# Optimization experiments

Hardware: AMD Instinct MI355X
Metric: run time of the kernel (lower is better)

The kernel has to match this reference:

```python
import jax, jax.numpy as jnp
import numpy as np

B1, B2, D = 8192, 8192, 128


def _cdist(d1, d2):
    # L2 distance matrix via the |a|^2 + |b|^2 - 2ab expansion (GEMM-dominant).
    d1_sq = jnp.sum(d1 * d1, axis=1, keepdims=True)          # (B1, 1)
    d2_sq = jnp.sum(d2 * d2, axis=1, keepdims=True)          # (B2, 1)
    dm = d1_sq + d2_sq.T - 2.0 * (d1 @ d2.T)                 # (B1, B2)
    return jnp.sqrt(jnp.clip(dm, 0.0))


def setup_inputs() -> dict:
    key = jax.random.key(0)
    k1, k2 = jax.random.split(key)
    desc1 = jax.random.normal(k1, (B1, D), dtype=jnp.float32)
    desc2 = jax.random.normal(k2, (B2, D), dtype=jnp.float32)
    return {"desc1": desc1, "desc2": desc2}


def reference(desc1, desc2):
    # DescriptorMatcher(match_mode='nn'): nearest neighbor in desc2 for each desc1.
    dm = _cdist(desc1, desc2)                                # (B1, B2)
    idxs_in_2 = jnp.argmin(dm, axis=1)                       # (B1,)
    match_dists = jnp.take_along_axis(dm, idxs_in_2[:, None], axis=1)  # (B1, 1)
    idxs_in_1 = jnp.arange(dm.shape[0], dtype=jnp.int64 if jax.config.jax_enable_x64 else jnp.int32)
    matches_idxs = jnp.stack([idxs_in_1, idxs_in_2.astype(idxs_in_1.dtype)], axis=1)  # (B1, 2)
    return match_dists, matches_idxs
```

## Files before the change

kernel.cpp:

```cpp
#include <hip/hip_runtime.h>
#include <cstdint>

#define NB1 8192
#define NB2 8192
#define DDIM 128
#define KROW 256
#define NKITER 12

using half8   = __attribute__((ext_vector_type(8))) _Float16;
using half4   = __attribute__((ext_vector_type(4))) _Float16;
using float4v = __attribute__((ext_vector_type(4))) float;

typedef __attribute__((address_space(3))) void       lds_void;
typedef const __attribute__((address_space(1))) void glb_void;

__device__ inline unsigned long long packkey(float v, int j) {
  unsigned u = __float_as_uint(v);
  u = (u & 0x80000000u) ? ~u : (u | 0x80000000u);
  return ((unsigned long long)u << 32) | (unsigned)j;
}

__device__ __forceinline__ int a_src(int kt) { return (kt < 8) ? kt : kt - 8; }
__device__ __forceinline__ int b_src(int kt) { return (kt < 4) ? kt : kt - 4; }

__global__ __launch_bounds__(256) void convert_kernel(
    const float* __restrict__ d1, const float* __restrict__ d2,
    _Float16* __restrict__ A2, _Float16* __restrict__ B2,
    float* __restrict__ asq, float* __restrict__ bsq,
    unsigned long long* __restrict__ packed) {
  int gid  = blockIdx.x * 256 + threadIdx.x;
  int wv   = gid >> 6;
  int lane = gid & 63;
  int rowc = 2 * wv + (lane >> 5);
  bool isA = rowc < NB1;
  const float* src = isA ? d1 : d2;
  int row = isA ? rowc : rowc - NB1;
  int k4  = (lane & 31) * 4;

  float4 v = *(const float4*)&src[row * DDIM + k4];
  _Float16 h0 = (_Float16)v.x, h1 = (_Float16)v.y;
  _Float16 h2 = (_Float16)v.z, h3 = (_Float16)v.w;
  half4 hh = {h0, h1, h2, h3};
  half4 ll = {(_Float16)(v.x - (float)h0), (_Float16)(v.y - (float)h1),
              (_Float16)(v.z - (float)h2), (_Float16)(v.w - (float)h3)};

  _Float16* dst = (isA ? A2 : B2) + (size_t)row * KROW;
  *(half4*)&dst[k4]       = hh;
  *(half4*)&dst[128 + k4] = ll;

  float s = v.x * v.x + v.y * v.y + v.z * v.z + v.w * v.w;
  #pragma unroll
  for (int off = 16; off > 0; off >>= 1) s += __shfl_xor(s, off, 64);
  if ((lane & 31) == 0) (isA ? asq : bsq)[row] = s;

  if (gid < NB1) packed[gid] = 0xFFFFFFFFFFFFFFFFull;
}

__global__ __launch_bounds__(256, 3) void mfma_match_kernel(
    const _Float16* __restrict__ A2, const _Float16* __restrict__ B2,
    const float* __restrict__ bsq, unsigned long long* __restrict__ packed) {
  __shared__ unsigned long long smem[2 * 128 * 17];
  _Float16* Asb = (_Float16*)smem;
  _Float16* Bsb = (_Float16*)smem + 8192;

  const int t    = threadIdx.x;
  const int lane = t & 63;
  const int wid  = t >> 6;
  const int wm = wid >> 1, wn = wid & 1;
  const int lx = lane & 15, q = lane >> 4;

  const int id = blockIdx.x;
  const int xc = id & 7, kk = id >> 3;
  const int bx = ((kk >> 3) & 7) * 8 + xc;
  const int by = (kk & 7) + ((kk >> 6) & 7) * 8;
  const int row0 = bx * 128, col0 = by * 128;

  const int sA   = wid * 2;
  const int rloc = lane >> 2;
  const int qch  = ((lane & 3) - (rloc >> 1)) & 3;
  const int rA0  = sA * 16 + rloc;
  const int kofs = qch * 8;

  float4v acc[4][4];
  #pragma unroll
  for (int r = 0; r < 4; ++r)
    #pragma unroll
    for (int c = 0; c < 4; ++c) acc[r][c] = (float4v){0.f, 0.f, 0.f, 0.f};

  float bq[4]; int jc[4];
  #pragma unroll
  for (int c = 0; c < 4; ++c) {
    jc[c] = col0 + wn * 64 + 16 * c + lx;
    bq[c] = bsq[jc[c]];
  }

  auto stage = [&](int kt, int buf) {
    const _Float16* ga =
        A2 + (size_t)(row0 + rA0) * KROW + a_src(kt) * 32 + kofs;
    __builtin_amdgcn_global_load_lds((glb_void*)ga,
        (lds_void*)(Asb + buf * 4096 + sA * 512), 16, 0, 0);
    __builtin_amdgcn_global_load_lds((glb_void*)(ga + 16 * KROW),
        (lds_void*)(Asb + buf * 4096 + (sA + 1) * 512), 16, 0, 0);
    const _Float16* gb =
        B2 + (size_t)(col0 + rA0) * KROW + b_src(kt) * 32 + kofs;
    __builtin_amdgcn_global_load_lds((glb_void*)gb,
        (lds_void*)(Bsb + buf * 4096 + sA * 512), 16, 0, 0);
    __builtin_amdgcn_global_load_lds((glb_void*)(gb + 16 * KROW),
        (lds_void*)(Bsb + buf * 4096 + (sA + 1) * 512), 16, 0, 0);
  };

  stage(0, 0);

  const int sw = ((q + (lx >> 1)) & 3) * 8;

  #pragma unroll
  for (int kt = 0; kt < NKITER; ++kt) {
    __syncthreads();
    if (kt < NKITER - 1) stage(kt + 1, (kt + 1) & 1);
    const _Float16* Ab = Asb + (kt & 1) * 4096;
    const _Float16* Bb = Bsb + (kt & 1) * 4096;
    half8 af[4], bf[4];
    #pragma unroll
    for (int r = 0; r < 4; ++r)
      af[r] = *(const half8*)&Ab[(wm * 64 + 16 * r + lx) * 32 + sw];
    #pragma unroll
    for (int c = 0; c < 4; ++c)
      bf[c] = *(const half8*)&Bb[(wn * 64 + 16 * c + lx) * 32 + sw];
    #pragma unroll
    for (int r = 0; r < 4; ++r)
      #pragma unroll
      for (int c = 0; c < 4; ++c)
        acc[r][c] = __builtin_amdgcn_mfma_f32_16x16x32_f16(
            af[r], bf[c], acc[r][c], 0, 0, 0);
  }

  __syncthreads();
  #pragma unroll
  for (int r = 0; r < 4; ++r) {
    #pragma unroll
    for (int reg = 0; reg < 4; ++reg) {
      float bv = 1e30f; int bj = 0;
      #pragma unroll
      for (int c = 0; c < 4; ++c) {
        float val = fmaf(-2.f, acc[r][c][reg], bq[c]);
        if (val < bv) { bv = val; bj = jc[c]; }
      }
      int mrow = wm * 64 + 16 * r + 4 * q + reg;
      smem[(wn * 128 + mrow) * 17 + lx] = packkey(bv, bj);
    }
  }
  __syncthreads();
  if (t < 128) {
    unsigned long long best = ~0ull;
    #pragma unroll
    for (int w = 0; w < 2; ++w)
      #pragma unroll
      for (int x = 0; x < 16; ++x) {
        unsigned long long k = smem[(w * 128 + t) * 17 + x];
        if (k < best) best = k;
      }
    atomicMin(&packed[row0 + t], best);
  }
}

__global__ __launch_bounds__(256) void out_kernel(
    const unsigned long long* __restrict__ packed,
    const float* __restrict__ asq, float* __restrict__ out) {
  int r = blockIdx.x * 256 + threadIdx.x;
  unsigned long long best = packed[r];
  unsigned u = (unsigned)(best >> 32);
  u = (u & 0x80000000u) ? (u & 0x7fffffffu) : ~u;
  float val  = __uint_as_float(u);
  float dist = sqrtf(fmaxf(asq[r] + val, 0.f));
  int j = (int)(unsigned)(best & 0xffffffffu);
  out[r]               = dist;
  out[NB1 + 2 * r]     = (float)r;
  out[NB1 + 2 * r + 1] = (float)j;
}

extern "C" void kernel_launch(void* const* d_in, const int* in_sizes, int n_in,
                              void* d_out, int out_size, void* d_ws, size_t ws_size,
                              hipStream_t stream) {
  const float* d1 = (const float*)d_in[0];
  const float* d2 = (const float*)d_in[1];
  float* out = (float*)d_out;

  char* w = (char*)d_ws;
  float* asq = (float*)w;
  float* bsq = (float*)(w + 32768);
  _Float16* A2 = (_Float16*)(w + 65536);
  _Float16* B2 = (_Float16*)(w + 65536 + 4194304);
  unsigned long long* packed =
      (unsigned long long*)(w + 65536 + 2 * 4194304);

  convert_kernel<<<(NB1 + NB2) / 8, 256, 0, stream>>>(
      d1, d2, A2, B2, asq, bsq, packed);

  mfma_match_kernel<<<(NB1 / 128) * (NB2 / 128), 256, 0, stream>>>(
      A2, B2, bsq, packed);

  out_kernel<<<NB1 / 256, 256, 0, stream>>>(packed, asq, out);
}
```

Baseline: 126.5 us.

## Enlarge GEMM tile to 256x256 with 512 threads and 4-stage LDS pipeline

The match kernel moves from 128x128 tiles with 4 waves to 256x256 tiles with 8 waves, each wave computing 64x128. The single double buffer becomes a four-buffer ring filled three stages ahead, gated by explicit vmcnt waits and raw barriers, and MFMA sections run at raised wave priority. The aim is higher operand reuse per byte loaded and better hiding of global-load latency. In exchange it needs 128KB of LDS and more accumulator registers per thread, which can lower occupancy, and the grid shrinks to 1024 blocks.

```diff
diff --git a/kernel.cpp b/kernel.cpp
--- a/kernel.cpp
+++ b/kernel.cpp
@@ -5,7 +5,7 @@
 #define NB2 8192
 #define DDIM 128
 #define KROW 256
-#define NKITER 12
+#define NSTEP 12
 
 using half8   = __attribute__((ext_vector_type(8))) _Float16;
 using half4   = __attribute__((ext_vector_type(4))) _Float16;
@@ -56,109 +56,115 @@
   if (gid < NB1) packed[gid] = 0xFFFFFFFFFFFFFFFFull;
 }
 
-__global__ __launch_bounds__(256, 3) void mfma_match_kernel(
+__global__ __launch_bounds__(512, 2) void mfma_match_kernel(
     const _Float16* __restrict__ A2, const _Float16* __restrict__ B2,
     const float* __restrict__ bsq, unsigned long long* __restrict__ packed) {
-  __shared__ unsigned long long smem[2 * 128 * 17];
-  _Float16* Asb = (_Float16*)smem;
-  _Float16* Bsb = (_Float16*)smem + 8192;
+  __shared__ unsigned long long smem[16384];
+  _Float16* S = (_Float16*)smem;
 
   const int t    = threadIdx.x;
   const int lane = t & 63;
   const int wid  = t >> 6;
-  const int wm = wid >> 1, wn = wid & 1;
-  const int lx = lane & 15, q = lane >> 4;
-
-  const int id = blockIdx.x;
-  const int xc = id & 7, kk = id >> 3;
-  const int bx = ((kk >> 3) & 7) * 8 + xc;
-  const int by = (kk & 7) + ((kk >> 6) & 7) * 8;
-  const int row0 = bx * 128, col0 = by * 128;
-
-  const int sA   = wid * 2;
-  const int rloc = lane >> 2;
-  const int qch  = ((lane & 3) - (rloc >> 1)) & 3;
-  const int rA0  = sA * 16 + rloc;
-  const int kofs = qch * 8;
-
-  float4v acc[4][4];
-  #pragma unroll
-  for (int r = 0; r < 4; ++r)
-    #pragma unroll
-    for (int c = 0; c < 4; ++c) acc[r][c] = (float4v){0.f, 0.f, 0.f, 0.f};
-
-  float bq[4]; int jc[4];
-  #pragma unroll
-  for (int c = 0; c < 4; ++c) {
-    jc[c] = col0 + wn * 64 + 16 * c + lx;
-    bq[c] = bsq[jc[c]];
-  }
+  const int wm   = wid >> 1;
+  const int wn   = wid & 1;
+  const int lx   = lane & 15, q = lane >> 4;
+
+  const int id  = blockIdx.x;
+  const int xcd = id & 7, kk = id >> 3;
+  const int bx = (xcd & 1) * 16 + (kk & 15);
+  const int by = (xcd >> 1) * 8 + (kk >> 4);
+  const int row0 = bx * 256, col0 = by * 256;
+
+  const int rstg  = t >> 2;
+  const int cslot = t & 3;
+
+  float4v acc[4][8];
+  #pragma unroll
+  for (int m = 0; m < 4; ++m)
+    #pragma unroll
+    for (int c = 0; c < 8; ++c) acc[m][c] = (float4v){0.f, 0.f, 0.f, 0.f};
+
+  const int jc0 = col0 + wn * 128 + lx;
+  float bq[8];
+  #pragma unroll
+  for (int c = 0; c < 8; ++c) bq[c] = bsq[jc0 + 16 * c];
 
   auto stage = [&](int kt, int buf) {
-    const _Float16* ga =
-        A2 + (size_t)(row0 + rA0) * KROW + a_src(kt) * 32 + kofs;
-    __builtin_amdgcn_global_load_lds((glb_void*)ga,
-        (lds_void*)(Asb + buf * 4096 + sA * 512), 16, 0, 0);
-    __builtin_amdgcn_global_load_lds((glb_void*)(ga + 16 * KROW),
-        (lds_void*)(Asb + buf * 4096 + (sA + 1) * 512), 16, 0, 0);
-    const _Float16* gb =
-        B2 + (size_t)(col0 + rA0) * KROW + b_src(kt) * 32 + kofs;
-    __builtin_amdgcn_global_load_lds((glb_void*)gb,
-        (lds_void*)(Bsb + buf * 4096 + sA * 512), 16, 0, 0);
-    __builtin_amdgcn_global_load_lds((glb_void*)(gb + 16 * KROW),
-        (lds_void*)(Bsb + buf * 4096 + (sA + 1) * 512), 16, 0, 0);
+    const int koA = a_src(kt) * 32, koB = b_src(kt) * 32;
+    #pragma unroll
+    for (int call = 0; call < 2; ++call) {
+      const int R  = call * 128 + rstg;
+      const int cc = (cslot - (R >> 1)) & 3;
+      const _Float16* ga = A2 + (size_t)(row0 + R) * KROW + koA + cc * 8;
+      __builtin_amdgcn_global_load_lds((glb_void*)ga,
+          (lds_void*)(S + buf * 16384 + call * 4096 + wid * 512), 16, 0, 0);
+      const _Float16* gb = B2 + (size_t)(col0 + R) * KROW + koB + cc * 8;
+      __builtin_amdgcn_global_load_lds((glb_void*)gb,
+          (lds_void*)(S + buf * 16384 + 8192 + call * 4096 + wid * 512), 16, 0, 0);
+    }
   };
 
-  stage(0, 0);
-
   const int sw = ((q + (lx >> 1)) & 3) * 8;
 
-  #pragma unroll
-  for (int kt = 0; kt < NKITER; ++kt) {
-    __syncthreads();
-    if (kt < NKITER - 1) stage(kt + 1, (kt + 1) & 1);
-    const _Float16* Ab = Asb + (kt & 1) * 4096;
-    const _Float16* Bb = Bsb + (kt & 1) * 4096;
-    half8 af[4], bf[4];
-    #pragma unroll
-    for (int r = 0; r < 4; ++r)
-      af[r] = *(const half8*)&Ab[(wm * 64 + 16 * r + lx) * 32 + sw];
-    #pragma unroll
-    for (int c = 0; c < 4; ++c)
-      bf[c] = *(const half8*)&Bb[(wn * 64 + 16 * c + lx) * 32 + sw];
-    #pragma unroll
-    for (int r = 0; r < 4; ++r)
+  auto compute = [&](int buf) {
+    const _Float16* Ab = S + buf * 16384;
+    const _Float16* Bb = Ab + 8192;
+    half8 af[4], bf[8];
+    #pragma unroll
+    for (int m = 0; m < 4; ++m)
+      af[m] = *(const half8*)&Ab[(wm * 64 + 16 * m + lx) * 32 + sw];
+    #pragma unroll
+    for (int c = 0; c < 8; ++c)
+      bf[c] = *(const half8*)&Bb[(wn * 128 + 16 * c + lx) * 32 + sw];
+    __builtin_amdgcn_s_setprio(1);
+    #pragma unroll
+    for (int m = 0; m < 4; ++m)
       #pragma unroll
-      for (int c = 0; c < 4; ++c)
-        acc[r][c] = __builtin_amdgcn_mfma_f32_16x16x32_f16(
-            af[r], bf[c], acc[r][c], 0, 0, 0);
-  }
+      for (int c = 0; c < 8; ++c)
+        acc[m][c] = __builtin_amdgcn_mfma_f32_16x16x32_f16(
+            af[m], bf[c], acc[m][c], 0, 0, 0);
+    __builtin_amdgcn_s_setprio(0);
+  };
+
+  stage(0, 0); stage(1, 1); stage(2, 2);
+
+#define STEP(K, N)                                                    \
+  do {                                                                \
+    asm volatile("s_waitcnt vmcnt(" #N ")" ::: "memory");             \
+    __builtin_amdgcn_s_barrier();                                     \
+    asm volatile("" ::: "memory");                                    \
+    if constexpr ((K) + 3 < NSTEP) stage((K) + 3, ((K) + 3) & 3);     \
+    compute((K) & 3);                                                 \
+  } while (0)
+
+  STEP(0, 8);  STEP(1, 8);  STEP(2, 8);  STEP(3, 8);
+  STEP(4, 8);  STEP(5, 8);  STEP(6, 8);  STEP(7, 8);
+  STEP(8, 8);  STEP(9, 8);  STEP(10, 4); STEP(11, 0);
+#undef STEP
 
   __syncthreads();
   #pragma unroll
-  for (int r = 0; r < 4; ++r) {
+  for (int m = 0; m < 4; ++m) {
     #pragma unroll
     for (int reg = 0; reg < 4; ++reg) {
       float bv = 1e30f; int bj = 0;
       #pragma unroll
-      for (int c = 0; c < 4; ++c) {
-        float val = fmaf(-2.f, acc[r][c][reg], bq[c]);
-        if (val < bv) { bv = val; bj = jc[c]; }
+      for (int c = 0; c < 8; ++c) {
+        float val = fmaf(-2.f, acc[m][c][reg], bq[c]);
+        if (val < bv) { bv = val; bj = jc0 + 16 * c; }
       }
-      int mrow = wm * 64 + 16 * r + 4 * q + reg;
-      smem[(wn * 128 + mrow) * 17 + lx] = packkey(bv, bj);
+      const int mrow = wm * 64 + 16 * m + 4 * q + reg;
+      smem[mrow * 33 + wn * 16 + lx] = packkey(bv, bj);
     }
   }
   __syncthreads();
-  if (t < 128) {
+  if (t < 256) {
     unsigned long long best = ~0ull;
     #pragma unroll
-    for (int w = 0; w < 2; ++w)
-      #pragma unroll
-      for (int x = 0; x < 16; ++x) {
-        unsigned long long k = smem[(w * 128 + t) * 17 + x];
-        if (k < best) best = k;
-      }
+    for (int c = 0; c < 32; ++c) {
+      unsigned long long kx = smem[t * 33 + ((2 * t + c) & 31)];
+      if (kx < best) best = kx;
+    }
     atomicMin(&packed[row0 + t], best);
   }
 }
@@ -196,7 +202,7 @@
   convert_kernel<<<(NB1 + NB2) / 8, 256, 0, stream>>>(
       d1, d2, A2, B2, asq, bsq, packed);
 
-  mfma_match_kernel<<<(NB1 / 128) * (NB2 / 128), 256, 0, stream>>>(
+  mfma_match_kernel<<<(NB1 / 256) * (NB2 / 256), 512, 0, stream>>>(
       A2, B2, bsq, packed);
 
   out_kernel<<<NB1 / 256, 256, 0, stream>>>(packed, asq, out);
```

Result: faster. 117.8 us (-6.9%).
